# Kernel optimization log

Hardware: AMD Instinct MI355X
Metric: run time of the kernel (lower is better)

## Reference

```python
import jax, jax.numpy as jnp
from jax import lax
import numpy as np

B, C, H, W = 4, 256, 64, 64
CQK = C // 8  # 32


def conv3x3(x, w, b):
    # x: [B,C_in,H,W], w: [C_out,C_in,3,3], b: [C_out]
    y = lax.conv_general_dilated(x, w, window_strides=(1, 1), padding='SAME',
                                 dimension_numbers=('NCHW', 'OIHW', 'NCHW'))
    return y + b[None, :, None, None]


def setup_inputs() -> dict:
    key = jax.random.key(0)
    ks = jax.random.split(key, 8)
    scale = 0.02
    return {
        'x': jax.random.normal(ks[0], (B, C, H, W), dtype=jnp.float32),
        'wq': jax.random.normal(ks[1], (CQK, C, 3, 3), dtype=jnp.float32) * scale,
        'bq': jax.random.normal(ks[2], (CQK,), dtype=jnp.float32) * scale,
        'wk': jax.random.normal(ks[3], (CQK, C, 3, 3), dtype=jnp.float32) * scale,
        'bk': jax.random.normal(ks[4], (CQK,), dtype=jnp.float32) * scale,
        'wv': jax.random.normal(ks[5], (C, C, 3, 3), dtype=jnp.float32) * scale,
        'bv': jax.random.normal(ks[6], (C,), dtype=jnp.float32) * scale,
        'gamma': jax.random.normal(ks[7], (1,), dtype=jnp.float32) * scale,
    }


def reference(x, wq, bq, wk, bk, wv, bv, gamma):
    b, c, h, w = x.shape
    n = h * w
    # Q: [B, N, C//8]  (permute(0,2,1) of the flattened conv output)
    q = conv3x3(x, wq, bq).reshape(b, -1, n).transpose(0, 2, 1)
    # K: [B, C//8, N]
    k = conv3x3(x, wk, bk).reshape(b, -1, n)
    # s: [B, N_q, N_k]
    s = jnp.einsum('bqd,bdk->bqk', q, k)
    # NOTE: original uses Softmax(dim=-2), i.e. over the QUERY axis
    attn_T = jax.nn.softmax(s, axis=-2)
    # V: [B, C, N]
    v = conv3x3(x, wv, bv).reshape(b, c, n)
    # o = bmm(V, attn_T): [B, C, N]
    o = jnp.einsum('bcq,bqk->bck', v, attn_T).reshape(b, c, h, w)
    return x + gamma * o
```

## Files before the change

kernel.cpp:

```cpp
#include <hip/hip_runtime.h>
#include <cstddef>

#define N_PIX 4096
#define HW 64
#define LOG2E 1.4426950408889634f
#define SHIFT2 28.8539008177793f

typedef __attribute__((ext_vector_type(8))) short bf16x8;
typedef __attribute__((ext_vector_type(4))) float f32x4;

static __device__ __forceinline__ unsigned short f2bf(float f) {
    union { float f; unsigned u; } v; v.f = f;
    unsigned r = v.u + 0x7fffu + ((v.u >> 16) & 1u);
    return (unsigned short)(r >> 16);
}
static __device__ __forceinline__ float bf2f(unsigned short s) {
    union { unsigned u; float f; } v; v.u = (unsigned)s << 16;
    return v.f;
}
static __device__ __forceinline__ unsigned pack_bf16_trunc(float lo, float hi) {
    union { float f; unsigned u; } a, b; a.f = hi; b.f = lo;
    return __builtin_amdgcn_perm(a.u, b.u, 0x07060302u);
}

__global__ __launch_bounds__(256) void x_transpose(
    const float* __restrict__ x, unsigned short* __restrict__ xbf)
{
    __shared__ unsigned short Ts[64][72];
    const int tid = threadIdx.x;
    const int px0 = blockIdx.x * 64, ci0 = blockIdx.y * 64, b = blockIdx.z;
    const float* xb = x + ((size_t)b * 256 + ci0) * N_PIX;

#pragma unroll
    for (int r = 0; r < 4; ++r) {
        int c = r * 16 + (tid >> 4);
        int p4 = (tid & 15) * 4;
        float4 v = *(const float4*)&xb[(size_t)c * N_PIX + px0 + p4];
        Ts[c][p4 + 0] = f2bf(v.x);
        Ts[c][p4 + 1] = f2bf(v.y);
        Ts[c][p4 + 2] = f2bf(v.z);
        Ts[c][p4 + 3] = f2bf(v.w);
    }
    __syncthreads();
#pragma unroll
    for (int r = 0; r < 2; ++r) {
        int id = tid * 2 + r;
        int p = id >> 3, c8 = (id & 7) * 8;
        ushort4 lo, hi;
        lo.x = Ts[c8 + 0][p]; lo.y = Ts[c8 + 1][p];
        lo.z = Ts[c8 + 2][p]; lo.w = Ts[c8 + 3][p];
        hi.x = Ts[c8 + 4][p]; hi.y = Ts[c8 + 5][p];
        hi.z = Ts[c8 + 6][p]; hi.w = Ts[c8 + 7][p];
        size_t off = ((size_t)b * N_PIX + px0 + p) * 256 + ci0 + c8;
        *(ushort4*)&xbf[off]     = lo;
        *(ushort4*)&xbf[off + 4] = hi;
    }
}

__global__ __launch_bounds__(256) void w_transform(
    const float* __restrict__ wq, const float* __restrict__ wk,
    const float* __restrict__ wv, unsigned short* __restrict__ wAll)
{
    int gid = blockIdx.x * 256 + threadIdx.x;
    if (gid >= 72 * 320 * 4) return;
    int part = gid & 3;
    int m = (gid >> 2) % 320;
    int kb = gid / 1280;
    int t = kb >> 3;
    int ci0 = (kb & 7) * 32 + part * 8;
    const float* src; int co; float sc = 1.f;
    if (m < 256)      { src = wv; co = m; }
    else if (m < 288) { src = wq; co = m - 256; sc = LOG2E; }
    else              { src = wk; co = m - 288; }
    ushort4 lo, hi;
    lo.x = f2bf(sc * src[((size_t)co * 256 + ci0 + 0) * 9 + t]);
    lo.y = f2bf(sc * src[((size_t)co * 256 + ci0 + 1) * 9 + t]);
    lo.z = f2bf(sc * src[((size_t)co * 256 + ci0 + 2) * 9 + t]);
    lo.w = f2bf(sc * src[((size_t)co * 256 + ci0 + 3) * 9 + t]);
    hi.x = f2bf(sc * src[((size_t)co * 256 + ci0 + 4) * 9 + t]);
    hi.y = f2bf(sc * src[((size_t)co * 256 + ci0 + 5) * 9 + t]);
    hi.z = f2bf(sc * src[((size_t)co * 256 + ci0 + 6) * 9 + t]);
    hi.w = f2bf(sc * src[((size_t)co * 256 + ci0 + 7) * 9 + t]);
    size_t off = ((size_t)kb * 320 + m) * 32 + part * 8;
    *(ushort4*)&wAll[off]     = lo;
    *(ushort4*)&wAll[off + 4] = hi;
}

__global__ __launch_bounds__(256) void conv_gemm_all(
    const unsigned short* __restrict__ xbf, const unsigned short* __restrict__ wAll,
    const float* __restrict__ bq, const float* __restrict__ bk,
    const float* __restrict__ bv,
    unsigned short* __restrict__ vbf, unsigned short* __restrict__ qt,
    unsigned short* __restrict__ kt)
{
    const int tid = threadIdx.x;
    const int w = tid >> 6, lane = tid & 63, quad = lane >> 4, l15 = lane & 15;
    const int px0 = blockIdx.x * 128;
    const int ct  = blockIdx.y;
    const int b   = blockIdx.z;
    const int row0 = (ct < 4) ? ct * 64 : 256;

    __shared__ unsigned short Al[2][64 * 40];
    __shared__ unsigned short Bl[2][128 * 40];

    const unsigned short* xb = xbf + (size_t)b * N_PIX * 256;

    const int arow = tid >> 2, apart = tid & 3;
    const int brow = tid >> 1, bp0 = (tid & 1) * 2;
    const int py = (px0 + brow) >> 6, pxc = brow & 63;

    f32x4 acc[4][2];
#pragma unroll
    for (int cb = 0; cb < 4; ++cb)
#pragma unroll
        for (int jb = 0; jb < 2; ++jb) acc[cb][jb] = (f32x4){0.f, 0.f, 0.f, 0.f};

    auto load_pair = [&](int kb0, bf16x8* aR, bf16x8* bR) {
#pragma unroll
        for (int h = 0; h < 2; ++h) {
            int kb = kb0 + h;
            int t = kb >> 3, ci0 = (kb & 7) << 5;
            int dy = t / 3 - 1, dx = t - (t / 3) * 3 - 1;
            int gy = py + dy, gx = pxc + dx;
            bool valid = (unsigned)gy < 64u && (unsigned)gx < 64u;
            aR[h] = *(const bf16x8*)&wAll[((size_t)kb * 320 + row0 + arow) * 32 + apart * 8];
            if (valid) {
                const unsigned short* bsrc =
                    xb + ((size_t)(gy * 64 + gx) * 256 + ci0 + bp0 * 8);
                bR[2 * h + 0] = *(const bf16x8*)&bsrc[0];
                bR[2 * h + 1] = *(const bf16x8*)&bsrc[8];
            } else {
                bR[2 * h + 0] = (bf16x8){0,0,0,0,0,0,0,0};
                bR[2 * h + 1] = (bf16x8){0,0,0,0,0,0,0,0};
            }
        }
    };

    bf16x8 aR[2], bR[4], aN[2], bN[4];
    load_pair(0, aR, bR);

    for (int kp = 0; kp < 36; ++kp) {
        __syncthreads();
#pragma unroll
        for (int h = 0; h < 2; ++h) {
            *(bf16x8*)&Al[h][arow * 40 + apart * 8]     = aR[h];
            *(bf16x8*)&Bl[h][brow * 40 + bp0 * 8]       = bR[2 * h + 0];
            *(bf16x8*)&Bl[h][brow * 40 + (bp0 + 1) * 8] = bR[2 * h + 1];
        }
        __syncthreads();
        if (kp + 1 < 36) load_pair(2 * (kp + 1), aN, bN);

#pragma unroll
        for (int h = 0; h < 2; ++h) {
            bf16x8 af[4], bf[2];
#pragma unroll
            for (int cb = 0; cb < 4; ++cb)
                af[cb] = *(const bf16x8*)&Al[h][(cb * 16 + l15) * 40 + quad * 8];
#pragma unroll
            for (int jb = 0; jb < 2; ++jb)
                bf[jb] = *(const bf16x8*)&Bl[h][(w * 32 + jb * 16 + l15) * 40 + quad * 8];
#pragma unroll
            for (int cb = 0; cb < 4; ++cb)
#pragma unroll
                for (int jb = 0; jb < 2; ++jb)
                    acc[cb][jb] = __builtin_amdgcn_mfma_f32_16x16x32_bf16(
                        af[cb], bf[jb], acc[cb][jb], 0, 0, 0);
        }

#pragma unroll
        for (int h = 0; h < 2; ++h) aR[h] = aN[h];
#pragma unroll
        for (int r = 0; r < 4; ++r) bR[r] = bN[r];
    }

    if (ct < 4) {
#pragma unroll
        for (int cb = 0; cb < 4; ++cb) {
            int c = ct * 64 + cb * 16 + quad * 4;
#pragma unroll
            for (int r = 0; r < 4; ++r) {
                float bias = bv[c + r];
#pragma unroll
                for (int jb = 0; jb < 2; ++jb) {
                    int px = px0 + w * 32 + jb * 16 + l15;
                    vbf[((size_t)b * 256 + c + r) * N_PIX + px] = f2bf(acc[cb][jb][r] + bias);
                }
            }
        }
    } else {
#pragma unroll
        for (int cb = 0; cb < 4; ++cb) {
            int cl = cb * 16 + quad * 4;
#pragma unroll
            for (int r = 0; r < 4; ++r) {
                int c = cl + r;
                float bias = (c < 32) ? bq[c] * LOG2E : bk[c - 32];
#pragma unroll
                for (int jb = 0; jb < 2; ++jb) {
                    int px = px0 + w * 32 + jb * 16 + l15;
                    unsigned short val = f2bf(acc[cb][jb][r] + bias);
                    if (c < 32)
                        qt[((size_t)b * N_PIX + px) * 32 + c] = val;
                    else
                        kt[((size_t)b * N_PIX + px) * 32 + (c - 32)] = val;
                }
            }
        }
    }
}

__global__ __launch_bounds__(256, 2) void fused_attn_mfma(
    const unsigned short* __restrict__ qt, const unsigned short* __restrict__ kt,
    const unsigned short* __restrict__ vbf,
    unsigned short* __restrict__ Abuf, float* __restrict__ lbuf, int iRange)
{
    const int tid  = threadIdx.x;
    const int w    = tid >> 6;
    const int lane = tid & 63;
    const int quad = lane >> 4;
    const int l15  = lane & 15;
    const int j0   = blockIdx.x * 128;
    const int b    = blockIdx.y;
    const int sp   = blockIdx.z;
    const int iBeg = sp * iRange;
    const int NI   = iRange / 64;

    const unsigned short* qtb = qt + (size_t)b * N_PIX * 32;
    const unsigned short* ktb = kt + (size_t)b * N_PIX * 32;
    const unsigned short* vb  = vbf + (size_t)b * 256 * N_PIX;

    __shared__ unsigned Pfrag[2][4096];
    __shared__ float lred[4][128];

    bf16x8 kf[8];
#pragma unroll
    for (int jb = 0; jb < 8; ++jb)
        kf[jb] = *(const bf16x8*)&ktb[((size_t)(j0 + jb * 16 + l15)) * 32 + quad * 8];

    f32x4 acc[4][8];
#pragma unroll
    for (int cb = 0; cb < 4; ++cb)
#pragma unroll
        for (int jb = 0; jb < 8; ++jb)
            acc[cb][jb] = (f32x4){0.f, 0.f, 0.f, 0.f};

    float lpart[8] = {0.f, 0.f, 0.f, 0.f, 0.f, 0.f, 0.f, 0.f};

    const int wFrag = w >> 1;
    const int wL    = ((w & 1) << 5) + ((quad >> 1) << 4) + l15;
    const int wEl2  = (quad & 1) << 1;

    bf16x8 va[2][4];

    auto s_phase = [&](bf16x8 qa, int buf) {
#pragma unroll
        for (int jb = 0; jb < 8; ++jb) {
            f32x4 s = __builtin_amdgcn_mfma_f32_16x16x32_bf16(
                qa, kf[jb], (f32x4){-SHIFT2, -SHIFT2, -SHIFT2, -SHIFT2}, 0, 0, 0);
            float p0 = __builtin_amdgcn_exp2f(s[0]);
            float p1 = __builtin_amdgcn_exp2f(s[1]);
            float p2 = __builtin_amdgcn_exp2f(s[2]);
            float p3 = __builtin_amdgcn_exp2f(s[3]);
            lpart[jb] += (p0 + p1) + (p2 + p3);
            unsigned u0 = pack_bf16_trunc(p0, p1);
            unsigned u1 = pack_bf16_trunc(p2, p3);
            unsigned base = (((jb << 1) + wFrag) * 64 + wL) * 4 + wEl2;
            Pfrag[buf][base]     = u0;
            Pfrag[buf][base + 1] = u1;
        }
    };

    auto load_qa = [&](int i0) {
        return *(const bf16x8*)&qtb[((size_t)(i0 + w * 16 + l15)) * 32 + quad * 8];
    };
    auto load_va = [&](int i0) {
#pragma unroll
        for (int ks = 0; ks < 2; ++ks)
#pragma unroll
            for (int cb = 0; cb < 4; ++cb)
                va[ks][cb] = *(const bf16x8*)&vb[((size_t)(w * 64 + cb * 16 + l15)) * N_PIX
                                                 + i0 + ks * 32 + quad * 8];
    };

    load_va(iBeg);
    s_phase(load_qa(iBeg), 0);

    for (int n = 0; n < NI; ++n) {
        __syncthreads();
        const bool hasN = (n + 1 < NI);
        const int inext = iBeg + (n + 1) * 64;
        bf16x8 qaN;
        if (hasN) qaN = load_qa(inext);

#pragma unroll
        for (int ks = 0; ks < 2; ++ks) {
            bf16x8 pb[8];
#pragma unroll
            for (int jb = 0; jb < 8; ++jb)
                pb[jb] = *(const bf16x8*)&Pfrag[n & 1][(((jb << 1) + ks) * 64 + lane) * 4];
#pragma unroll
            for (int cb = 0; cb < 4; ++cb)
#pragma unroll
                for (int jb = 0; jb < 8; ++jb)
                    acc[cb][jb] = __builtin_amdgcn_mfma_f32_16x16x32_bf16(
                        va[ks][cb], pb[jb], acc[cb][jb], 0, 0, 0);
        }

        if (hasN) {
            load_va(inext);
            s_phase(qaN, (n + 1) & 1);
        }
    }

#pragma unroll
    for (int jb = 0; jb < 8; ++jb) {
        float v = lpart[jb];
        v += __shfl_xor(v, 16, 64);
        v += __shfl_xor(v, 32, 64);
        lpart[jb] = v;
    }
    if (lane < 16) {
#pragma unroll
        for (int jb = 0; jb < 8; ++jb)
            lred[w][jb * 16 + l15] = lpart[jb];
    }
    __syncthreads();
    if (tid < 128) {
        float s = lred[0][tid] + lred[1][tid] + lred[2][tid] + lred[3][tid];
        lbuf[((size_t)sp * 4 + b) * N_PIX + j0 + tid] = s;
    }

    unsigned short* Ab = Abuf + ((size_t)sp * 4 + b) * 256 * N_PIX;
#pragma unroll
    for (int cb = 0; cb < 4; ++cb) {
        int c = w * 64 + cb * 16 + quad * 4;
#pragma unroll
        for (int jb = 0; jb < 8; ++jb) {
            int j = j0 + jb * 16 + l15;
#pragma unroll
            for (int r = 0; r < 4; ++r)
                Ab[(size_t)(c + r) * N_PIX + j] = f2bf(acc[cb][jb][r]);
        }
    }
}

__global__ __launch_bounds__(256) void combine_kernel(
    const unsigned short* __restrict__ A, const float* __restrict__ L,
    const float* __restrict__ x, const float* __restrict__ gamma,
    float* __restrict__ out, int split)
{
    const size_t CH = (size_t)4 * 256 * N_PIX;
    size_t flat = ((size_t)blockIdx.x * 256 + threadIdx.x) * 8;
    int j = (int)(flat & (N_PIX - 1));
    int b = (int)(flat >> 20);

    float a[8] = {0.f, 0.f, 0.f, 0.f, 0.f, 0.f, 0.f, 0.f};
    float l[8] = {0.f, 0.f, 0.f, 0.f, 0.f, 0.f, 0.f, 0.f};
    for (int s = 0; s < split; ++s) {
        ushort4 av0 = *(const ushort4*)&A[flat + (size_t)s * CH];
        ushort4 av1 = *(const ushort4*)&A[flat + (size_t)s * CH + 4];
        a[0] += bf2f(av0.x); a[1] += bf2f(av0.y); a[2] += bf2f(av0.z); a[3] += bf2f(av0.w);
        a[4] += bf2f(av1.x); a[5] += bf2f(av1.y); a[6] += bf2f(av1.z); a[7] += bf2f(av1.w);
        float4 l0 = *(const float4*)&L[((size_t)s * 4 + b) * N_PIX + j];
        float4 l1 = *(const float4*)&L[((size_t)s * 4 + b) * N_PIX + j + 4];
        l[0] += l0.x; l[1] += l0.y; l[2] += l0.z; l[3] += l0.w;
        l[4] += l1.x; l[5] += l1.y; l[6] += l1.z; l[7] += l1.w;
    }
    float g = gamma[0];
    float4 x0 = *(const float4*)&x[flat];
    float4 x1 = *(const float4*)&x[flat + 4];
    float4 o0, o1;
    o0.x = x0.x + g * a[0] / l[0];
    o0.y = x0.y + g * a[1] / l[1];
    o0.z = x0.z + g * a[2] / l[2];
    o0.w = x0.w + g * a[3] / l[3];
    o1.x = x1.x + g * a[4] / l[4];
    o1.y = x1.y + g * a[5] / l[5];
    o1.z = x1.z + g * a[6] / l[6];
    o1.w = x1.w + g * a[7] / l[7];
    *(float4*)&out[flat]     = o0;
    *(float4*)&out[flat + 4] = o1;
}

extern "C" void kernel_launch(void* const* d_in, const int* in_sizes, int n_in,
                              void* d_out, int out_size, void* d_ws, size_t ws_size,
                              hipStream_t stream)
{
    const float* x     = (const float*)d_in[0];
    const float* wq    = (const float*)d_in[1];
    const float* bq    = (const float*)d_in[2];
    const float* wk    = (const float*)d_in[3];
    const float* bk    = (const float*)d_in[4];
    const float* wv    = (const float*)d_in[5];
    const float* bv    = (const float*)d_in[6];
    const float* gamma = (const float*)d_in[7];
    float* out = (float*)d_out;

    const size_t szQTel  = (size_t)4 * N_PIX * 32;
    const size_t szVBFel = (size_t)4 * 256 * N_PIX;
    const size_t szXBFel = (size_t)4 * N_PIX * 256;
    const size_t szWel   = (size_t)72 * 320 * 32;
    const size_t fixedB  = (2 * szQTel + szVBFel + szXBFel + szWel) * 2;

    int split = 4;
    while (split > 1) {
        size_t need = fixedB
                    + (size_t)split * 4 * 256 * N_PIX * 2
                    + (size_t)split * 4 * N_PIX * 4;
        if (need <= ws_size) break;
        split >>= 1;
    }

    unsigned short* Abuf = (unsigned short*)d_ws;
    float* lbuf = (float*)(Abuf + (size_t)split * 4 * 256 * N_PIX);
    unsigned short* qt   = (unsigned short*)(lbuf + (size_t)split * 4 * N_PIX);
    unsigned short* kt   = qt + szQTel;
    unsigned short* vbf  = kt + szQTel;
    unsigned short* xbf  = vbf + szVBFel;
    unsigned short* wAll = xbf + szXBFel;

    x_transpose<<<dim3(N_PIX / 64, 4, 4), 256, 0, stream>>>(x, xbf);
    w_transform<<<dim3((72 * 320 * 4 + 255) / 256), 256, 0, stream>>>(wq, wk, wv, wAll);

    conv_gemm_all<<<dim3(N_PIX / 128, 5, 4), 256, 0, stream>>>(
        xbf, wAll, bq, bk, bv, vbf, qt, kt);

    fused_attn_mfma<<<dim3(N_PIX / 128, 4, split), 256, 0, stream>>>(
        qt, kt, vbf, Abuf, lbuf, N_PIX / split);

    combine_kernel<<<dim3((4 * 256 * N_PIX) / (256 * 8)), 256, 0, stream>>>(
        Abuf, lbuf, x, gamma, out, split);
}
```

Measured before the change: 188.7 us.

## Read conv weights directly from global and double-buffer B tile in LDS

Weight A-fragments in the conv GEMM are now loaded straight from global memory (L1/L2 cached) into MFMA operands, so the A LDS staging is gone. The B (input pixel) tile moves to a double-buffered LDS layout, which needs one barrier per iteration instead of two, with the store for the next stage placed after the MFMAs. The load pattern for B also changes (split by channel half instead of row pairs). In exchange, A fragments are fetched redundantly by every wave from global memory, which adds latency and cache traffic to the inner loop.

```diff
diff --git a/kernel.cpp b/kernel.cpp
--- a/kernel.cpp
+++ b/kernel.cpp
@@ -98,15 +98,14 @@
     const int px0 = blockIdx.x * 128;
     const int ct  = blockIdx.y;
     const int b   = blockIdx.z;
-    const int row0 = (ct < 4) ? ct * 64 : 256;
-
-    __shared__ unsigned short Al[2][64 * 40];
-    __shared__ unsigned short Bl[2][128 * 40];
+    const int row0 = ct * 64;
+
+    __shared__ unsigned short Bl[2 * 2 * 128 * 40];
 
     const unsigned short* xb = xbf + (size_t)b * N_PIX * 256;
 
-    const int arow = tid >> 2, apart = tid & 3;
-    const int brow = tid >> 1, bp0 = (tid & 1) * 2;
+    const int brow  = tid & 127;
+    const int bpart = tid >> 7;
     const int py = (px0 + brow) >> 6, pxc = brow & 63;
 
     f32x4 acc[4][2];
@@ -115,7 +114,7 @@
 #pragma unroll
         for (int jb = 0; jb < 2; ++jb) acc[cb][jb] = (f32x4){0.f, 0.f, 0.f, 0.f};
 
-    auto load_pair = [&](int kb0, bf16x8* aR, bf16x8* bR) {
+    auto load_b = [&](int kb0, bf16x8* bR) {
 #pragma unroll
         for (int h = 0; h < 2; ++h) {
             int kb = kb0 + h;
@@ -123,42 +122,46 @@
             int dy = t / 3 - 1, dx = t - (t / 3) * 3 - 1;
             int gy = py + dy, gx = pxc + dx;
             bool valid = (unsigned)gy < 64u && (unsigned)gx < 64u;
-            aR[h] = *(const bf16x8*)&wAll[((size_t)kb * 320 + row0 + arow) * 32 + apart * 8];
             if (valid) {
-                const unsigned short* bsrc =
-                    xb + ((size_t)(gy * 64 + gx) * 256 + ci0 + bp0 * 8);
-                bR[2 * h + 0] = *(const bf16x8*)&bsrc[0];
-                bR[2 * h + 1] = *(const bf16x8*)&bsrc[8];
+                const unsigned short* s =
+                    xb + ((size_t)(gy * 64 + gx) * 256 + ci0 + bpart * 8);
+                bR[2 * h + 0] = *(const bf16x8*)&s[0];
+                bR[2 * h + 1] = *(const bf16x8*)&s[16];
             } else {
                 bR[2 * h + 0] = (bf16x8){0,0,0,0,0,0,0,0};
                 bR[2 * h + 1] = (bf16x8){0,0,0,0,0,0,0,0};
             }
         }
     };
-
-    bf16x8 aR[2], bR[4], aN[2], bN[4];
-    load_pair(0, aR, bR);
+    auto store_b = [&](int buf, const bf16x8* bR) {
+#pragma unroll
+        for (int h = 0; h < 2; ++h) {
+            *(bf16x8*)&Bl[buf * 10240 + h * 5120 + brow * 40 + bpart * 8]       = bR[2 * h + 0];
+            *(bf16x8*)&Bl[buf * 10240 + h * 5120 + brow * 40 + (bpart + 2) * 8] = bR[2 * h + 1];
+        }
+    };
+
+    bf16x8 bN[4];
+    load_b(0, bN);
+    store_b(0, bN);
 
     for (int kp = 0; kp < 36; ++kp) {
         __syncthreads();
+        const bool hasN = (kp + 1 < 36);
+        if (hasN) load_b(2 * (kp + 1), bN);
+
 #pragma unroll
         for (int h = 0; h < 2; ++h) {
-            *(bf16x8*)&Al[h][arow * 40 + apart * 8]     = aR[h];
-            *(bf16x8*)&Bl[h][brow * 40 + bp0 * 8]       = bR[2 * h + 0];
-            *(bf16x8*)&Bl[h][brow * 40 + (bp0 + 1) * 8] = bR[2 * h + 1];
-        }
-        __syncthreads();
-        if (kp + 1 < 36) load_pair(2 * (kp + 1), aN, bN);
-
-#pragma unroll
-        for (int h = 0; h < 2; ++h) {
+            int kb = 2 * kp + h;
             bf16x8 af[4], bf[2];
 #pragma unroll
             for (int cb = 0; cb < 4; ++cb)
-                af[cb] = *(const bf16x8*)&Al[h][(cb * 16 + l15) * 40 + quad * 8];
+                af[cb] = *(const bf16x8*)&wAll[((size_t)kb * 320 + row0 + cb * 16 + l15) * 32
+                                               + quad * 8];
 #pragma unroll
             for (int jb = 0; jb < 2; ++jb)
-                bf[jb] = *(const bf16x8*)&Bl[h][(w * 32 + jb * 16 + l15) * 40 + quad * 8];
+                bf[jb] = *(const bf16x8*)&Bl[(kp & 1) * 10240 + h * 5120
+                                             + (w * 32 + jb * 16 + l15) * 40 + quad * 8];
 #pragma unroll
             for (int cb = 0; cb < 4; ++cb)
 #pragma unroll
@@ -167,10 +170,7 @@
                         af[cb], bf[jb], acc[cb][jb], 0, 0, 0);
         }
 
-#pragma unroll
-        for (int h = 0; h < 2; ++h) aR[h] = aN[h];
-#pragma unroll
-        for (int r = 0; r < 4; ++r) bR[r] = bN[r];
+        if (hasN) store_b((kp + 1) & 1, bN);
     }
 
     if (ct < 4) {
```

New measurement: 235.2 us. 1.25x slower.
